# Kernel tuning notes

Measured on AMD Instinct MI355X. Metric: run time of the kernel, lower is better.

The kernel has to match this reference:

```python
import jax, jax.numpy as jnp
import numpy as np


def _conv1x1(X, W, b):
    # X: [B,C,H,W], W: [Cout,Cin], b: [Cout] -> [B,Cout,H,W]
    return jnp.einsum('oc,bchw->bohw', W, X) + b[None, :, None, None]


def setup_inputs() -> dict:
    key = jax.random.key(0)
    ks = jax.random.split(key, 7)
    B, C, H, W = 8, 512, 32, 32
    scale = 1.0 / np.sqrt(C)
    return {
        'X': jax.random.normal(ks[0], (B, C, H, W), dtype=jnp.float32),
        'W_phi': jax.random.normal(ks[1], (C, C), dtype=jnp.float32) * scale,
        'b_phi': jnp.zeros((C,), dtype=jnp.float32),
        'W_theta': jax.random.normal(ks[2], (C, C), dtype=jnp.float32) * scale,
        'b_theta': jnp.zeros((C,), dtype=jnp.float32),
        'W_beta': jax.random.normal(ks[3], (C, C), dtype=jnp.float32) * scale,
        'b_beta': jnp.zeros((C,), dtype=jnp.float32),
    }


def reference(X, W_phi, b_phi, W_theta, b_theta, W_beta, b_beta):
    B, C, H, W = X.shape
    N = H * W
    phi = _conv1x1(X, W_phi, b_phi).reshape(B, -1, N)      # [B,Co,N]
    theta = _conv1x1(X, W_theta, b_theta).reshape(B, -1, N)  # [B,Co,N]
    beta = _conv1x1(X, W_beta, b_beta).reshape(B, -1, N)    # [B,Co,N]
    # attention over spatial positions: scores [B,N,N], row-softmax
    A = jax.nn.softmax(jnp.einsum('bcn,bcm->bnm', phi, theta), axis=-1)
    Z = jnp.einsum('bcn,bnm->bcm', beta, A)                 # [B,Co,N]
    return Z.reshape(B, -1, H, W) + X
```

## Files before the change

kernel.cpp:

```cpp
#include <hip/hip_runtime.h>

typedef __bf16 bf16_t;
typedef __bf16 bf16x4 __attribute__((ext_vector_type(4)));
typedef __bf16 bf16x8 __attribute__((ext_vector_type(8)));
typedef _Float16 f16_t;
typedef _Float16 f16x4 __attribute__((ext_vector_type(4)));
typedef _Float16 f16x8 __attribute__((ext_vector_type(8)));
typedef float  f32x4  __attribute__((ext_vector_type(4)));

#define BK 64
#define BATCH 8
#define CDIM 512
#define NSP 1024
#define SOFF 90.0f


__device__ __forceinline__ void gl2lds16(const void* g, void* l) {
    __builtin_amdgcn_global_load_lds(
        (const __attribute__((address_space(1))) void*)g,
        (__attribute__((address_space(3))) void*)l, 16, 0, 0);
}

template<typename T, int NW, int ROWS>
__device__ __forceinline__ void stageRx64(const T* __restrict__ src, int ld, T* dst) {
    int lane = threadIdx.x & 63;
    int wave = threadIdx.x >> 6;
    constexpr int SPW = (ROWS / 8) / NW;
    int colsw = ((lane & 7) ^ (lane >> 3)) << 3;
#pragma unroll
    for (int c = 0; c < SPW; ++c) {
        int seg = wave * SPW + c;
        int row = (seg << 3) + (lane >> 3);
        gl2lds16(src + (size_t)row * ld + colsw, dst + (seg << 9));
    }
}

__device__ __forceinline__ f32x4 mfma_op(f16x8 a, f16x8 b, f32x4 c) {
    return __builtin_amdgcn_mfma_f32_16x16x32_f16(a, b, c, 0, 0, 0);
}
__device__ __forceinline__ f32x4 mfma_op(bf16x8 a, bf16x8 b, f32x4 c) {
    return __builtin_amdgcn_mfma_f32_16x16x32_bf16(a, b, c, 0, 0, 0);
}

template<typename VT, typename T, int K>
__device__ __forceinline__ void gemm128_ring(const T* __restrict__ A, int lda,
                                             const T* __restrict__ B, int ldb,
                                             T* sA, T* sB, f32x4 acc[4][4]) {
    int lane = threadIdx.x & 63;
    int wave = threadIdx.x >> 6;
    int wr = (wave >> 1) << 6;
    int wc = (wave & 1) << 6;
    int fr = lane & 15;
    int q  = lane >> 4;
    constexpr int HALF = 128 * BK;
    constexpr int NH = K / BK;

    stageRx64<T, 4, 128>(A, lda, sA);
    stageRx64<T, 4, 128>(B, ldb, sB);
    __builtin_amdgcn_sched_barrier(0);
    stageRx64<T, 4, 128>(A + BK, lda, sA + HALF);
    stageRx64<T, 4, 128>(B + BK, ldb, sB + HALF);
    __builtin_amdgcn_sched_barrier(0);

#pragma unroll
    for (int h = 0; h < NH; ++h) {
        if (h < NH - 1) asm volatile("s_waitcnt vmcnt(8)" ::: "memory");
        else            asm volatile("s_waitcnt vmcnt(0)" ::: "memory");
        __builtin_amdgcn_s_barrier();
        const T* pA = sA + (h & 1) * HALF;
        const T* pB = sB + (h & 1) * HALF;
#pragma unroll
        for (int kk = 0; kk < 2; ++kk) {
            int sc = ((((kk << 2) + q) ^ (fr & 7)) << 3);
            VT a[4], b[4];
#pragma unroll
            for (int i = 0; i < 4; ++i)
                a[i] = *reinterpret_cast<const VT*>(pA + (wr + i*16 + fr)*BK + sc);
#pragma unroll
            for (int j = 0; j < 4; ++j)
                b[j] = *reinterpret_cast<const VT*>(pB + (wc + j*16 + fr)*BK + sc);
#pragma unroll
            for (int mi = 0; mi < 4; ++mi)
#pragma unroll
                for (int ni = 0; ni < 4; ++ni)
                    acc[mi][ni] = mfma_op(a[mi], b[ni], acc[mi][ni]);
        }
        __builtin_amdgcn_s_barrier();
        if (h + 2 < NH) {
            stageRx64<T, 4, 128>(A + (h + 2) * BK, lda, sA + (h & 1) * HALF);
            stageRx64<T, 4, 128>(B + (h + 2) * BK, ldb, sB + (h & 1) * HALF);
            __builtin_amdgcn_sched_barrier(0);
        }
    }
}

__device__ __forceinline__ void zero44(f32x4 acc[4][4]) {
#pragma unroll
    for (int i = 0; i < 4; i++)
#pragma unroll
        for (int j = 0; j < 4; j++)
#pragma unroll
            for (int e = 0; e < 4; e++) acc[i][j][e] = 0.0f;
}

__global__ __launch_bounds__(256)
void prep_kernel(const float* __restrict__ X, const float* __restrict__ Wp,
                 const float* __restrict__ Wt, const float* __restrict__ Wb,
                 f16_t* __restrict__ Xt, f16_t* __restrict__ W16) {
    int z = blockIdx.z;
    int tx = threadIdx.x;
    int ty = threadIdx.y;
    if (z == 8) {
        int g = (blockIdx.y * 32 + blockIdx.x) * 256 + ty * 8 + tx;
        if (g < 98304) {
            int i = g << 3;
            int r = i >> 9, c = i & 511;
            const float* src = (r < 512) ? (Wp + ((size_t)r << 9))
                             : (r < 1024) ? (Wt + ((size_t)(r - 512) << 9))
                                          : (Wb + ((size_t)(r - 1024) << 9));
            float4 v0 = *reinterpret_cast<const float4*>(src + c);
            float4 v1 = *reinterpret_cast<const float4*>(src + c + 4);
            f16x8 o;
            o[0]=(f16_t)v0.x; o[1]=(f16_t)v0.y; o[2]=(f16_t)v0.z; o[3]=(f16_t)v0.w;
            o[4]=(f16_t)v1.x; o[5]=(f16_t)v1.y; o[6]=(f16_t)v1.z; o[7]=(f16_t)v1.w;
            *reinterpret_cast<f16x8*>(W16 + i) = o;
        }
        return;
    }
    __shared__ float tile[32][33];
    const float* x = X + (size_t)z * CDIM * NSP;
    int c0 = blockIdx.y * 32, n0 = blockIdx.x * 32;
    float4 v = *reinterpret_cast<const float4*>(x + (size_t)(c0 + ty) * NSP + n0 + tx * 4);
    tile[ty][tx * 4 + 0] = v.x;
    tile[ty][tx * 4 + 1] = v.y;
    tile[ty][tx * 4 + 2] = v.z;
    tile[ty][tx * 4 + 3] = v.w;
    __syncthreads();
    f16x4 o;
#pragma unroll
    for (int i = 0; i < 4; ++i) o[i] = (f16_t)tile[tx * 4 + i][ty];
    *reinterpret_cast<f16x4*>(Xt + (size_t)z * NSP * CDIM + (size_t)(n0 + ty) * CDIM + c0 + tx * 4) = o;
}

__global__ __launch_bounds__(256, 2)
void conv_pt_kernel(const f16_t* __restrict__ Xt, const f16_t* __restrict__ W16,
                    const float* __restrict__ bias_phi, const float* __restrict__ bias_theta,
                    f16_t* __restrict__ phiH, f16_t* __restrict__ thH) {
    __shared__ alignas(16) f16_t sA[2 * 128 * BK], sB[2 * 128 * BK];
    int b = blockIdx.x;
    int j = blockIdx.y;
    int n0 = (j >> 3) << 7;
    int col0 = (j & 7) << 7;
    f32x4 acc[4][4];
    zero44(acc);
    gemm128_ring<f16x8, f16_t, CDIM>(Xt + ((size_t)b * NSP + n0) * CDIM, CDIM,
                                     W16 + (size_t)col0 * CDIM, CDIM, sA, sB, acc);

    int lane = threadIdx.x & 63;
    int wave = threadIdx.x >> 6;
    int wr = (wave >> 1) << 6, wc = (wave & 1) << 6;
    int fr = lane & 15, q4 = ((lane >> 4) << 2);

    bool isPhi = (col0 < 512);
    const float* bias = isPhi ? bias_phi : bias_theta;
    f16_t* dh = (isPhi ? phiH : thH) + (size_t)b * NSP * CDIM;
    int oc0 = col0 & 511;
#pragma unroll
    for (int mi = 0; mi < 4; mi++)
#pragma unroll
        for (int ni = 0; ni < 4; ni++) {
            int col = oc0 + wc + ni * 16 + fr;
            float bv = bias[col];
#pragma unroll
            for (int e = 0; e < 4; e++) {
                int row = n0 + wr + mi * 16 + q4 + e;
                dh[(size_t)row * CDIM + col] = (f16_t)(acc[mi][ni][e] + bv);
            }
        }
}

__global__ __launch_bounds__(256, 2)
void sgemm_beta_kernel(const f16_t* __restrict__ Xt, const f16_t* __restrict__ W16,
                       const f16_t* __restrict__ phiH, const f16_t* __restrict__ thH,
                       const float* __restrict__ bias_beta,
                       bf16_t* __restrict__ Et, float* __restrict__ psum,
                       bf16_t* __restrict__ betaB) {
    __shared__ alignas(16) f16_t sA[2 * 128 * BK], sB[2 * 128 * BK];
    int b = blockIdx.x;
    int j = blockIdx.y;
    int lane = threadIdx.x & 63;
    int wave = threadIdx.x >> 6;
    int wr = (wave >> 1) << 6, wc = (wave & 1) << 6;
    int fr = lane & 15, q4 = ((lane >> 4) << 2);
    f32x4 acc[4][4];
    zero44(acc);

    if (j < 64) {
        int n0 = (j >> 3) << 7, m0 = (j & 7) << 7;
        gemm128_ring<f16x8, f16_t, CDIM>(phiH + ((size_t)b * NSP + n0) * CDIM, CDIM,
                                         thH + ((size_t)b * NSP + m0) * CDIM, CDIM,
                                         sA, sB, acc);
        bf16_t* et = Et + (size_t)b * NSP * NSP;
        float p[4][4];
#pragma unroll
        for (int mi = 0; mi < 4; mi++)
#pragma unroll
            for (int e = 0; e < 4; e++) p[mi][e] = 0.0f;
#pragma unroll
        for (int mi = 0; mi < 4; mi++)
#pragma unroll
            for (int ni = 0; ni < 4; ni++) {
                int col = m0 + wc + ni * 16 + fr;
                int rowb = n0 + wr + mi * 16 + q4;
                bf16x4 v;
#pragma unroll
                for (int e = 0; e < 4; e++) {
                    float ev = __expf(acc[mi][ni][e] - SOFF);
                    p[mi][e] += ev;
                    v[e] = (bf16_t)ev;
                }
                *reinterpret_cast<bf16x4*>(et + (size_t)col * NSP + rowb) = v;
            }
#pragma unroll
        for (int mi = 0; mi < 4; mi++)
#pragma unroll
            for (int e = 0; e < 4; e++) {
#pragma unroll
                for (int off = 1; off < 16; off <<= 1)
                    p[mi][e] += __shfl_xor(p[mi][e], off);
            }
        if ((lane & 15) == 0) {
            int pidx = ((j & 7) << 1) + (wc >> 6);
            float* ps = psum + ((size_t)b * 16 + pidx) * NSP;
#pragma unroll
            for (int mi = 0; mi < 4; mi++)
#pragma unroll
                for (int e = 0; e < 4; e++)
                    ps[n0 + wr + mi * 16 + q4 + e] = p[mi][e];
        }
    } else {
        int j2 = j - 64;
        int nb = j2 >> 2, cb = j2 & 3;
        int n0 = nb << 7;
        gemm128_ring<f16x8, f16_t, CDIM>(Xt + ((size_t)b * NSP + n0) * CDIM, CDIM,
                                         W16 + (size_t)(1024 + cb * 128) * CDIM, CDIM,
                                         sA, sB, acc);
        bf16_t* dst = betaB + (size_t)b * CDIM * NSP;
#pragma unroll
        for (int mi = 0; mi < 4; mi++)
#pragma unroll
            for (int ni = 0; ni < 4; ni++) {
                int c = cb * 128 + wc + ni * 16 + fr;
                float bv = bias_beta[c];
                int rowb = n0 + wr + mi * 16 + q4;
                bf16x4 v;
#pragma unroll
                for (int e = 0; e < 4; e++) v[e] = (bf16_t)(acc[mi][ni][e] + bv);
                *reinterpret_cast<bf16x4*>(dst + (size_t)c * NSP + rowb) = v;
            }
    }
}

__global__ __launch_bounds__(512, 4)
void zgemm_kernel(const bf16_t* __restrict__ betaB, const bf16_t* __restrict__ Et,
                  const float* __restrict__ psum, const float* __restrict__ X,
                  float* __restrict__ out) {
    __shared__ float rs[NSP];
    __shared__ alignas(16) bf16_t sA[2 * 64 * BK];
    __shared__ alignas(16) bf16_t sB[2 * 128 * BK];
    int b = blockIdx.x;
    int m0 = blockIdx.y * 128;
    int c0 = blockIdx.z * 64;
    int tid = threadIdx.x;

#pragma unroll
    for (int i = 0; i < 2; ++i) {
        int n = i * 512 + tid;
        float s = 0.f;
#pragma unroll
        for (int pp = 0; pp < 16; ++pp) s += psum[((size_t)b * 16 + pp) * NSP + n];
        rs[n] = 1.0f / s;
    }
    __syncthreads();

    int lane = tid & 63, wave = tid >> 6;
    int fr = lane & 15, q = lane >> 4, q4 = (lane >> 4) << 2;
    int wr = (wave >> 2) << 5;
    int wc = (wave & 3) << 5;
    int ar = lane >> 3, ac = lane & 7;
    int acs = ac ^ ar;

    const bf16_t* A = betaB + ((size_t)b * CDIM + c0) * NSP;
    const bf16_t* B = Et + ((size_t)b * NSP + m0) * NSP;
    f32x4 acc[2][2];
#pragma unroll
    for (int i = 0; i < 2; i++)
#pragma unroll
        for (int jj = 0; jj < 2; jj++)
#pragma unroll
            for (int e = 0; e < 4; e++) acc[i][jj][e] = 0.0f;

    int row = (wave << 3) + ar;

    for (int k0 = 0; k0 < NSP; k0 += 2 * BK) {
        stageRx64<bf16_t, 8, 128>(B + k0, NSP, sB);
        __builtin_amdgcn_sched_barrier(0);
        bf16x8 v0 = *reinterpret_cast<const bf16x8*>(A + (size_t)row * NSP + k0 + ac * 8);
        bf16x8 v1 = *reinterpret_cast<const bf16x8*>(A + (size_t)row * NSP + k0 + BK + ac * 8);
        __builtin_amdgcn_sched_barrier(0);
        stageRx64<bf16_t, 8, 128>(B + k0 + BK, NSP, sB + 128 * BK);
        __builtin_amdgcn_sched_barrier(0);
#pragma unroll
        for (int h = 0; h < 2; ++h) {
            int kh = k0 + h * BK;
            float4 r0v = *reinterpret_cast<const float4*>(&rs[kh + ac * 8]);
            float4 r1v = *reinterpret_cast<const float4*>(&rs[kh + ac * 8 + 4]);
            bf16x8 v = h ? v1 : v0;
            bf16x8 o;
            o[0] = (bf16_t)((float)v[0] * r0v.x);
            o[1] = (bf16_t)((float)v[1] * r0v.y);
            o[2] = (bf16_t)((float)v[2] * r0v.z);
            o[3] = (bf16_t)((float)v[3] * r0v.w);
            o[4] = (bf16_t)((float)v[4] * r1v.x);
            o[5] = (bf16_t)((float)v[5] * r1v.y);
            o[6] = (bf16_t)((float)v[6] * r1v.z);
            o[7] = (bf16_t)((float)v[7] * r1v.w);
            *reinterpret_cast<bf16x8*>(sA + h * 64 * BK + (wave << 9) + ar * 64 + acs * 8) = o;
        }
        asm volatile("s_waitcnt vmcnt(2) lgkmcnt(0)" ::: "memory");
        __builtin_amdgcn_s_barrier();
#pragma unroll
        for (int h = 0; h < 2; ++h) {
            const bf16_t* pA = sA + h * 64 * BK;
            const bf16_t* pB = sB + h * 128 * BK;
#pragma unroll
            for (int kk = 0; kk < 2; ++kk) {
                int sc = ((((kk << 2) + q) ^ (fr & 7)) << 3);
                bf16x8 a[2], bbv[2];
#pragma unroll
                for (int i = 0; i < 2; ++i)
                    a[i] = *reinterpret_cast<const bf16x8*>(pA + (wr + i*16 + fr)*BK + sc);
#pragma unroll
                for (int jj = 0; jj < 2; ++jj)
                    bbv[jj] = *reinterpret_cast<const bf16x8*>(pB + (wc + jj*16 + fr)*BK + sc);
#pragma unroll
                for (int mi = 0; mi < 2; ++mi)
#pragma unroll
                    for (int ni = 0; ni < 2; ++ni)
                        acc[mi][ni] = mfma_op(a[mi], bbv[ni], acc[mi][ni]);
            }
            if (h == 0) {
                asm volatile("s_waitcnt vmcnt(0)" ::: "memory");
                __builtin_amdgcn_s_barrier();
            }
        }
        __builtin_amdgcn_s_barrier();
    }

    const float* xs = X + (size_t)b * CDIM * NSP;
    float* dst = out + (size_t)b * CDIM * NSP;
#pragma unroll
    for (int mi = 0; mi < 2; mi++)
#pragma unroll
        for (int ni = 0; ni < 2; ni++) {
            int col = m0 + wc + ni * 16 + fr;
#pragma unroll
            for (int e = 0; e < 4; e++) {
                int rowo = c0 + wr + mi * 16 + q4 + e;
                size_t idx = (size_t)rowo * NSP + col;
                dst[idx] = acc[mi][ni][e] + xs[idx];
            }
        }
}

extern "C" void kernel_launch(void* const* d_in, const int* in_sizes, int n_in,
                              void* d_out, int out_size, void* d_ws, size_t ws_size,
                              hipStream_t stream) {
    const float* X  = (const float*)d_in[0];
    const float* Wp = (const float*)d_in[1];
    const float* bp = (const float*)d_in[2];
    const float* Wt = (const float*)d_in[3];
    const float* bt = (const float*)d_in[4];
    const float* Wb = (const float*)d_in[5];
    const float* bb = (const float*)d_in[6];
    float* out = (float*)d_out;

    char* ws = (char*)d_ws;
    size_t off = 0;
    auto alloc = [&](size_t bytes) -> char* {
        char* p = ws + off;
        off += (bytes + 255) & ~(size_t)255;
        return p;
    };

    const size_t BNC2 = (size_t)BATCH * NSP * CDIM * 2;
    f16_t*  Xt16  = (f16_t*)alloc(BNC2);
    f16_t*  W16   = (f16_t*)alloc((size_t)1536 * 512 * 2);
    f16_t*  phiH  = (f16_t*)alloc(BNC2);
    f16_t*  thH   = (f16_t*)alloc(BNC2);
    bf16_t* betaB = (bf16_t*)alloc(BNC2);
    bf16_t* Et    = (bf16_t*)alloc((size_t)BATCH * NSP * NSP * 2);
    float*  psum  = (float*)alloc((size_t)BATCH * 16 * NSP * 4);

    prep_kernel<<<dim3(32, 16, 9), dim3(8, 32), 0, stream>>>(X, Wp, Wt, Wb, Xt16, W16);
    conv_pt_kernel<<<dim3(8, 64), dim3(256), 0, stream>>>(Xt16, W16, bp, bt, phiH, thH);
    sgemm_beta_kernel<<<dim3(8, 96), dim3(256), 0, stream>>>(Xt16, W16, phiH, thH,
                                                             bb, Et, psum, betaB);
    zgemm_kernel<<<dim3(8, 8, 8), dim3(512), 0, stream>>>(betaB, Et, psum, X, out);

    (void)in_sizes; (void)n_in; (void)out_size; (void)ws_size;
}
```

Measured before the change: 64.97 us.

## Software-pipeline the Z GEMM K-loop with double-buffered LDS prefetch

Restructures the final beta×E GEMM loop from a per-128 K step that loads both halves and then computes into a rolling double-buffered pipeline. While one 64-wide K tile is consumed, the next tile's B rows and A values are already staged or in flight. The intent is to overlap global-to-LDS loads with MFMA work instead of stalling at each K step. The loop is fully unrolled, and the vmcnt wait counts must match the outstanding loads, which adds register and code-size pressure.

New measurement: 65.64 us. Within noise of the previous version (+1.0%).

```diff
diff --git a/kernel.cpp b/kernel.cpp
--- a/kernel.cpp
+++ b/kernel.cpp
@@ -289,8 +289,9 @@
     int wc = (wave & 3) << 5;
     int ar = lane >> 3, ac = lane & 7;
     int acs = ac ^ ar;
-
-    const bf16_t* A = betaB + ((size_t)b * CDIM + c0) * NSP;
+    constexpr int NH = NSP / BK;
+
+    const bf16_t* Arow = betaB + ((size_t)b * CDIM + c0 + (wave << 3) + ar) * NSP;
     const bf16_t* B = Et + ((size_t)b * NSP + m0) * NSP;
     f32x4 acc[2][2];
 #pragma unroll
@@ -300,61 +301,72 @@
 #pragma unroll
             for (int e = 0; e < 4; e++) acc[i][jj][e] = 0.0f;
 
-    int row = (wave << 3) + ar;
-
-    for (int k0 = 0; k0 < NSP; k0 += 2 * BK) {
-        stageRx64<bf16_t, 8, 128>(B + k0, NSP, sB);
-        __builtin_amdgcn_sched_barrier(0);
-        bf16x8 v0 = *reinterpret_cast<const bf16x8*>(A + (size_t)row * NSP + k0 + ac * 8);
-        bf16x8 v1 = *reinterpret_cast<const bf16x8*>(A + (size_t)row * NSP + k0 + BK + ac * 8);
-        __builtin_amdgcn_sched_barrier(0);
-        stageRx64<bf16_t, 8, 128>(B + k0 + BK, NSP, sB + 128 * BK);
-        __builtin_amdgcn_sched_barrier(0);
-#pragma unroll
-        for (int h = 0; h < 2; ++h) {
-            int kh = k0 + h * BK;
-            float4 r0v = *reinterpret_cast<const float4*>(&rs[kh + ac * 8]);
-            float4 r1v = *reinterpret_cast<const float4*>(&rs[kh + ac * 8 + 4]);
-            bf16x8 v = h ? v1 : v0;
-            bf16x8 o;
-            o[0] = (bf16_t)((float)v[0] * r0v.x);
-            o[1] = (bf16_t)((float)v[1] * r0v.y);
-            o[2] = (bf16_t)((float)v[2] * r0v.z);
-            o[3] = (bf16_t)((float)v[3] * r0v.w);
-            o[4] = (bf16_t)((float)v[4] * r1v.x);
-            o[5] = (bf16_t)((float)v[5] * r1v.y);
-            o[6] = (bf16_t)((float)v[6] * r1v.z);
-            o[7] = (bf16_t)((float)v[7] * r1v.w);
-            *reinterpret_cast<bf16x8*>(sA + h * 64 * BK + (wave << 9) + ar * 64 + acs * 8) = o;
-        }
-        asm volatile("s_waitcnt vmcnt(2) lgkmcnt(0)" ::: "memory");
+    auto aload = [&](int h) -> bf16x8 {
+        return *reinterpret_cast<const bf16x8*>(Arow + h * BK + ac * 8);
+    };
+    auto scale_write = [&](bf16x8 v, int h) {
+        float4 r0v = *reinterpret_cast<const float4*>(&rs[h * BK + ac * 8]);
+        float4 r1v = *reinterpret_cast<const float4*>(&rs[h * BK + ac * 8 + 4]);
+        bf16x8 o;
+        o[0] = (bf16_t)((float)v[0] * r0v.x);
+        o[1] = (bf16_t)((float)v[1] * r0v.y);
+        o[2] = (bf16_t)((float)v[2] * r0v.z);
+        o[3] = (bf16_t)((float)v[3] * r0v.w);
+        o[4] = (bf16_t)((float)v[4] * r1v.x);
+        o[5] = (bf16_t)((float)v[5] * r1v.y);
+        o[6] = (bf16_t)((float)v[6] * r1v.z);
+        o[7] = (bf16_t)((float)v[7] * r1v.w);
+        *reinterpret_cast<bf16x8*>(sA + (h & 1) * 64 * BK + (wave << 9) + ar * 64 + acs * 8) = o;
+    };
+
+    bf16x8 va0 = aload(0);
+    __builtin_amdgcn_sched_barrier(0);
+    stageRx64<bf16_t, 8, 128>(B, NSP, sB);
+    __builtin_amdgcn_sched_barrier(0);
+    bf16x8 va1 = aload(1);
+    __builtin_amdgcn_sched_barrier(0);
+    stageRx64<bf16_t, 8, 128>(B + BK, NSP, sB + 128 * BK);
+    __builtin_amdgcn_sched_barrier(0);
+    scale_write(va0, 0);
+    scale_write(va1, 1);
+    __builtin_amdgcn_sched_barrier(0);
+
+    bf16x8 vnext;
+#pragma unroll
+    for (int h = 0; h < NH; ++h) {
+        if (h + 2 < NH) {
+            vnext = aload(h + 2);
+            __builtin_amdgcn_sched_barrier(0);
+        }
+        if (h + 2 < NH)      asm volatile("s_waitcnt vmcnt(3) lgkmcnt(0)" ::: "memory");
+        else if (h + 1 < NH) asm volatile("s_waitcnt vmcnt(2) lgkmcnt(0)" ::: "memory");
+        else                 asm volatile("s_waitcnt vmcnt(0) lgkmcnt(0)" ::: "memory");
         __builtin_amdgcn_s_barrier();
-#pragma unroll
-        for (int h = 0; h < 2; ++h) {
-            const bf16_t* pA = sA + h * 64 * BK;
-            const bf16_t* pB = sB + h * 128 * BK;
-#pragma unroll
-            for (int kk = 0; kk < 2; ++kk) {
-                int sc = ((((kk << 2) + q) ^ (fr & 7)) << 3);
-                bf16x8 a[2], bbv[2];
-#pragma unroll
-                for (int i = 0; i < 2; ++i)
-                    a[i] = *reinterpret_cast<const bf16x8*>(pA + (wr + i*16 + fr)*BK + sc);
-#pragma unroll
-                for (int jj = 0; jj < 2; ++jj)
-                    bbv[jj] = *reinterpret_cast<const bf16x8*>(pB + (wc + jj*16 + fr)*BK + sc);
-#pragma unroll
-                for (int mi = 0; mi < 2; ++mi)
-#pragma unroll
-                    for (int ni = 0; ni < 2; ++ni)
-                        acc[mi][ni] = mfma_op(a[mi], bbv[ni], acc[mi][ni]);
-            }
-            if (h == 0) {
-                asm volatile("s_waitcnt vmcnt(0)" ::: "memory");
-                __builtin_amdgcn_s_barrier();
-            }
+        const bf16_t* pA = sA + (h & 1) * 64 * BK;
+        const bf16_t* pB = sB + (h & 1) * 128 * BK;
+#pragma unroll
+        for (int kk = 0; kk < 2; ++kk) {
+            int sc = ((((kk << 2) + q) ^ (fr & 7)) << 3);
+            bf16x8 a[2], bbv[2];
+#pragma unroll
+            for (int i = 0; i < 2; ++i)
+                a[i] = *reinterpret_cast<const bf16x8*>(pA + (wr + i*16 + fr)*BK + sc);
+#pragma unroll
+            for (int jj = 0; jj < 2; ++jj)
+                bbv[jj] = *reinterpret_cast<const bf16x8*>(pB + (wc + jj*16 + fr)*BK + sc);
+#pragma unroll
+            for (int mi = 0; mi < 2; ++mi)
+#pragma unroll
+                for (int ni = 0; ni < 2; ++ni)
+                    acc[mi][ni] = mfma_op(a[mi], bbv[ni], acc[mi][ni]);
         }
         __builtin_amdgcn_s_barrier();
+        if (h + 2 < NH) {
+            stageRx64<bf16_t, 8, 128>(B + (h + 2) * BK, NSP, sB + (h & 1) * 128 * BK);
+            __builtin_amdgcn_sched_barrier(0);
+            scale_write(vnext, h + 2);
+            __builtin_amdgcn_sched_barrier(0);
+        }
     }
 
     const float* xs = X + (size_t)b * CDIM * NSP;
```
